# Performance work log

Hardware: AMD Instinct MI355X
Metric: run time of the kernel (lower is better)

Reference implementation:

```python
import jax, jax.numpy as jnp
import numpy as np

SR = 44100
K = 1.0 / SR                      # time step
LX = 0.5
MAX_OM = 10000.0 * 2.0 * np.pi    # fmax * 2pi
MIN_OM = 20.0 * 2.0 * np.pi
TAU0, TAU1 = 6.0, 1.0
OM2SQ = (2.0 * np.pi * 500.0) ** 2          # OmDamp2^2 (OmDamp1 = 0)
ALPHA = 3.0 * np.log(10.0) / OM2SQ * (OM2SQ / TAU0)   # = 3 ln10 / tau0
BETA = 3.0 * np.log(10.0) / OM2SQ * (1.0 / TAU1 - 1.0 / TAU0)
MU_SCALE, DMU_SCALE, T0MU_SCALE = 2.43, 0.002452, 0.004115
M_MAX = 80  # 80x80 = 6400 modes


def setup_inputs() -> dict:
    z = jnp.zeros((), dtype=jnp.float32)
    return {
        "mu_raw": z, "D_over_mu_raw": z, "T0_over_mu_raw": z,
        "Ly_raw": z, "xo_raw": z, "yo_raw": z,
        "num_samples": 22050,
    }


def _modal_ir(mu_raw, D_over_mu_raw, T0_over_mu_raw, Ly_raw, xo_raw, yo_raw, num_samples):
    sp, sg = jax.nn.softplus, jax.nn.sigmoid
    # physical parameters via differentiable bounds
    mu = (sp(mu_raw) + 1e-4) * MU_SCALE
    D_over_mu = (sp(D_over_mu_raw) + 1e-4) * DMU_SCALE
    T0_over_mu = (sp(T0_over_mu_raw) + 1e-4) * T0MU_SCALE
    Ly = 1.1 + (4.0 - 1.1) * sg(Ly_raw)
    xo = 0.49 * LX + (1.0 - 0.49) * LX * sg(xo_raw)
    yo = 0.51 * Ly + (1.0 - 0.51) * Ly * sg(yo_raw)
    xi = 0.1 * LX
    yi = 0.1 * Ly
    # mode grid [6400]
    idx = jnp.arange(1, M_MAX + 1, dtype=jnp.float32)
    gm, gn = jnp.meshgrid(idx, idx, indexing="ij")
    m, n = gm.ravel(), gn.ravel()
    g1 = (m * np.pi / LX) ** 2 + (n * np.pi / Ly) ** 2
    omega_sq = T0_over_mu * g1 + D_over_mu * g1 * g1
    omega = jnp.sqrt(jax.nn.relu(omega_sq))
    valid = ((omega <= MAX_OM) & (omega >= MIN_OM)).astype(omega.dtype)
    InW = jnp.cos(xi * np.pi * m / LX) * jnp.cos(yi * np.pi * n / Ly)
    OutW = jnp.cos(xo * np.pi * m / LX) * jnp.cos(yo * np.pi * n / Ly)
    sigma = ALPHA + BETA * omega ** 2
    ms = 0.25 * mu * LX * Ly
    P = OutW * InW * (K * K) * jnp.exp(-sigma * K) / ms * valid  # [modes]
    # time axis [T]
    t = jnp.arange(num_samples, dtype=jnp.float32)
    decay_env = jnp.exp(-sigma[:, None] * (t[None, :] - 1.0) * K)    # [modes, T]
    sine_num = jnp.sin(t[None, :] * omega[:, None] * K)              # [modes, T]
    sine_den = jnp.sin(omega * K) + 1e-8                             # [modes]
    mode_waveforms = P[:, None] * decay_env * (sine_num / sine_den[:, None])
    disp = jnp.sum(mode_waveforms, axis=0)                           # [T]
    peak = jnp.max(jnp.abs(disp)) + 1e-8
    return disp / peak


def reference(mu_raw, D_over_mu_raw, T0_over_mu_raw, Ly_raw, xo_raw, yo_raw, num_samples):
    return _modal_ir(mu_raw, D_over_mu_raw, T0_over_mu_raw, Ly_raw, xo_raw, yo_raw, num_samples)
```

## Files before the change

kernel.cpp:

```cpp
#include <hip/hip_runtime.h>
#include <math.h>

#define NMODES 6400
#define TB     128
#define MPT    10
#define NPAIR  5
#define MG     5
#define BATCH  6
#define TC     42

typedef float v2f __attribute__((ext_vector_type(2)));

static __device__ __forceinline__ float softplusf(float x) {
    return log1pf(expf(-fabsf(x))) + fmaxf(x, 0.0f);
}
static __device__ __forceinline__ float sigmoidf(float x) {
    return 1.0f / (1.0f + expf(-x));
}

__global__ void setup_zero_kernel(const float* __restrict__ mu_raw,
                                  const float* __restrict__ Dmu_raw,
                                  const float* __restrict__ T0mu_raw,
                                  const float* __restrict__ Ly_raw,
                                  const float* __restrict__ xo_raw,
                                  const float* __restrict__ yo_raw,
                                  float* __restrict__ wsA,
                                  float* __restrict__ wsW,
                                  float* __restrict__ wsS,
                                  float* __restrict__ wsCW,
                                  float* __restrict__ wsSW,
                                  unsigned int* __restrict__ peak,
                                  float* __restrict__ out, int T)
{
    int id = blockIdx.x * blockDim.x + threadIdx.x;
    int gsz = gridDim.x * blockDim.x;
    for (int i = id; i < T; i += gsz) out[i] = 0.0f;
    if (id == 0) *peak = 0u;
    if (id >= NMODES) return;

    const float KF   = 1.0f / 44100.0f;
    const float PI_F = (float)M_PI;
    const double om2sq = (2.0 * M_PI * 500.0) * (2.0 * M_PI * 500.0);
    const float ALPHA_F  = (float)(3.0 * M_LN10 / om2sq * (om2sq / 6.0));
    const float BETA_F   = (float)(3.0 * M_LN10 / om2sq * (1.0 - 1.0 / 6.0));
    const float MAX_OM_F = (float)(10000.0 * 2.0 * M_PI);
    const float MIN_OM_F = (float)(20.0 * 2.0 * M_PI);
    const float KK_F     = (float)((1.0 / 44100.0) * (1.0 / 44100.0));

    float mu   = (softplusf(mu_raw[0])   + 1e-4f) * 2.43f;
    float Dmu  = (softplusf(Dmu_raw[0])  + 1e-4f) * 0.002452f;
    float T0mu = (softplusf(T0mu_raw[0]) + 1e-4f) * 0.004115f;
    float Ly   = 1.1f + 2.9f * sigmoidf(Ly_raw[0]);
    float xo   = 0.245f + 0.255f * sigmoidf(xo_raw[0]);
    float yo   = __fadd_rn(__fmul_rn(0.51f, Ly),
                           __fmul_rn(__fmul_rn(0.49f, Ly), sigmoidf(yo_raw[0])));

    float mf = (float)(id / 80 + 1);
    float nf = (float)(id % 80 + 1);

    float am = __fmul_rn(__fmul_rn(mf, PI_F), 2.0f);
    float bn = __fdiv_rn(__fmul_rn(nf, PI_F), Ly);
    float g1 = __fadd_rn(__fmul_rn(am, am), __fmul_rn(bn, bn));
    float omega_sq = __fadd_rn(__fmul_rn(T0mu, g1),
                               __fmul_rn(__fmul_rn(Dmu, g1), g1));
    float omega = sqrtf(fmaxf(omega_sq, 0.0f));
    float valid = (omega <= MAX_OM_F && omega >= MIN_OM_F) ? 1.0f : 0.0f;

    float xi_pi = (float)(0.05 * M_PI);
    float yi = __fmul_rn(0.1f, Ly);
    float InW = __fmul_rn(
        cosf(__fmul_rn(__fmul_rn(xi_pi, mf), 2.0f)),
        cosf(__fdiv_rn(__fmul_rn(__fmul_rn(yi, PI_F), nf), Ly)));
    float OutW = __fmul_rn(
        cosf(__fmul_rn(__fmul_rn(__fmul_rn(xo, PI_F), mf), 2.0f)),
        cosf(__fdiv_rn(__fmul_rn(__fmul_rn(yo, PI_F), nf), Ly)));

    float sigma = __fadd_rn(ALPHA_F, __fmul_rn(BETA_F, __fmul_rn(omega, omega)));
    float ms = __fmul_rn(__fmul_rn(__fmul_rn(0.25f, mu), 0.5f), Ly);
    float P = __fmul_rn(
        __fdiv_rn(__fmul_rn(__fmul_rn(__fmul_rn(OutW, InW), KK_F),
                            expf(__fmul_rn(-sigma, KF))),
                  ms),
        valid);
    float den = __fadd_rn(sinf(__fmul_rn(omega, KF)), 1e-8f);
    float A = __fdiv_rn(P, den);

    const double Kd = 1.0 / 44100.0;
    double th = (double)omega * Kd;
    double dd = exp(-(double)sigma * Kd);
    wsA[id]  = A;
    wsW[id]  = omega;
    wsS[id]  = sigma;
    wsCW[id] = (float)(dd * cos(th));
    wsSW[id] = (float)(dd * sin(th));
}

__global__ __launch_bounds__(TB) void accum_kernel(
    const float* __restrict__ wsA,
    const float* __restrict__ wsW,
    const float* __restrict__ wsS,
    const float* __restrict__ wsCW,
    const float* __restrict__ wsSW,
    float* __restrict__ out, int T)
{
    __shared__ __align__(16) float lds[TC][TB + 2];

    const int tid  = threadIdx.x;
    const int t0   = blockIdx.x * TC;
    const int base = blockIdx.y * (TB * MPT);

    const float  KF     = 1.0f / 44100.0f;
    const double Kd     = 1.0 / 44100.0;
    const double TWO_PI = 6.283185307179586476925286766559;
    const double I2PI   = 0.15915494309189533576888376337251;

    v2f S[NPAIR], C[NPAIR], CW[NPAIR], SW[NPAIR];
    #pragma unroll
    for (int p = 0; p < NPAIR; ++p) {
        int m = base + p * (TB * 2) + tid * 2;
        CW[p] = *(const v2f*)(wsCW + m);
        SW[p] = *(const v2f*)(wsSW + m);
        v2f A  = *(const v2f*)(wsA + m);
        v2f w  = *(const v2f*)(wsW + m);
        v2f sg = *(const v2f*)(wsS + m);
        #pragma unroll
        for (int k = 0; k < 2; ++k) {
            double ph = (double)t0 * (double)w[k] * Kd;
            double q  = rint(ph * I2PI);
            float  r  = (float)fma(-q, TWO_PI, ph);
            float s0, c0;
            __sincosf(r, &s0, &c0);
            float env = A[k] * __expf(-sg[k] * (float)(t0 - 1) * KF);
            S[p][k] = env * s0;
            C[p][k] = env * c0;
        }
    }

    #pragma unroll 1
    for (int it = 0; it < TC; it += BATCH) {
        #pragma unroll
        for (int b = 0; b < BATCH; ++b) {
            v2f s01 = S[0] + S[1];
            v2f s23 = S[2] + S[3];
            v2f sp  = (s01 + s23) + S[4];
            lds[it + b][tid] = sp[0] + sp[1];
            #pragma unroll
            for (int p = 0; p < NPAIR; ++p) {
                v2f nS = __builtin_elementwise_fma(S[p], CW[p], C[p] * SW[p]);
                v2f nC = __builtin_elementwise_fma(C[p], CW[p], -(S[p] * SW[p]));
                S[p] = nS;
                C[p] = nC;
            }
        }
    }
    __syncthreads();

    const int wv   = tid >> 6;
    const int lane = tid & 63;
    if (lane < TC / 2) {
        int s = wv * (TC / 2) + lane;
        v2f z = {0.0f, 0.0f};
        #pragma unroll
        for (int r = 0; r < TB / 2; ++r)
            z += *(const v2f*)&lds[s][2 * r];
        int t = t0 + s;
        if (t < T) atomicAdd(&out[t], z[0] + z[1]);
    }
}

__global__ __launch_bounds__(256) void max_kernel(
    const float* __restrict__ out,
    unsigned int* __restrict__ peak, int T)
{
    __shared__ float red[4];
    int i = blockIdx.x * 256 + threadIdx.x;
    float mx = 0.0f;
    if (2 * i + 1 < T) {
        v2f v = *(const v2f*)(out + 2 * i);
        mx = fmaxf(fabsf(v[0]), fabsf(v[1]));
    } else if (2 * i < T) {
        mx = fabsf(out[2 * i]);
    }
    #pragma unroll
    for (int off = 32; off > 0; off >>= 1)
        mx = fmaxf(mx, __shfl_xor(mx, off, 64));
    int lane = threadIdx.x & 63, wvx = threadIdx.x >> 6;
    if (lane == 0) red[wvx] = mx;
    __syncthreads();
    if (threadIdx.x == 0) {
        float m = fmaxf(fmaxf(red[0], red[1]), fmaxf(red[2], red[3]));
        atomicMax(peak, __float_as_uint(m));
    }
}

__global__ __launch_bounds__(256) void div_kernel(
    float* __restrict__ out, const unsigned int* __restrict__ peak, int T)
{
    float pk = __uint_as_float(*peak) + 1e-8f;
    int i = blockIdx.x * 256 + threadIdx.x;
    if (2 * i + 1 < T) {
        v2f v = *(const v2f*)(out + 2 * i);
        v[0] = __fdiv_rn(v[0], pk);
        v[1] = __fdiv_rn(v[1], pk);
        *(v2f*)(out + 2 * i) = v;
    } else if (2 * i < T) {
        out[2 * i] = __fdiv_rn(out[2 * i], pk);
    }
}

extern "C" void kernel_launch(void* const* d_in, const int* in_sizes, int n_in,
                              void* d_out, int out_size, void* d_ws, size_t ws_size,
                              hipStream_t stream)
{
    const float* mu   = (const float*)d_in[0];
    const float* Dmu  = (const float*)d_in[1];
    const float* T0mu = (const float*)d_in[2];
    const float* Lyr  = (const float*)d_in[3];
    const float* xor_ = (const float*)d_in[4];
    const float* yor_ = (const float*)d_in[5];
    float* out = (float*)d_out;

    float* ws   = (float*)d_ws;
    float* wsA  = ws;
    float* wsW  = ws + NMODES;
    float* wsS  = ws + 2 * NMODES;
    float* wsCW = ws + 3 * NMODES;
    float* wsSW = ws + 4 * NMODES;
    unsigned int* peak = (unsigned int*)(ws + 5 * NMODES);

    int T = out_size;
    int tchunks = (T + TC - 1) / TC;
    int npairs  = (T + 1) / 2;
    int nblk    = (npairs + 255) / 256;

    setup_zero_kernel<<<(NMODES + 255) / 256, 256, 0, stream>>>(
        mu, Dmu, T0mu, Lyr, xor_, yor_, wsA, wsW, wsS, wsCW, wsSW, peak, out, T);
    accum_kernel<<<dim3(tchunks, MG), TB, 0, stream>>>(wsA, wsW, wsS, wsCW, wsSW, out, T);
    max_kernel<<<nblk, 256, 0, stream>>>(out, peak, T);
    div_kernel<<<nblk, 256, 0, stream>>>(out, peak, T);
}
```

Baseline: 92.41 us.

## Fuse setup, accumulation, max and normalize into one cooperative kernel

Replaces the four separate launches (setup/zero, accumulate, max, divide) with a single cooperative persistent kernel using grid.sync between phases. The accumulate tiles (about 2625) are spread across a fixed 1024-block grid in a grid-stride loop. The aim is to remove per-launch overhead and the gaps between kernels. In exchange it adds grid-wide barriers and load imbalance, since the tile count does not divide evenly over 1024 blocks. Cooperative launch also requires all 1024 blocks to be resident at once.

```diff
diff --git a/kernel.cpp b/kernel.cpp
--- a/kernel.cpp
+++ b/kernel.cpp
@@ -1,4 +1,5 @@
 #include <hip/hip_runtime.h>
+#include <hip/hip_cooperative_groups.h>
 #include <math.h>
 
 #define NMODES 6400
@@ -8,6 +9,9 @@
 #define MG     5
 #define BATCH  6
 #define TC     42
+#define GRID   1024
+
+namespace cg = cooperative_groups;
 
 typedef float v2f __attribute__((ext_vector_type(2)));
 
@@ -18,193 +22,187 @@
     return 1.0f / (1.0f + expf(-x));
 }
 
-__global__ void setup_zero_kernel(const float* __restrict__ mu_raw,
-                                  const float* __restrict__ Dmu_raw,
-                                  const float* __restrict__ T0mu_raw,
-                                  const float* __restrict__ Ly_raw,
-                                  const float* __restrict__ xo_raw,
-                                  const float* __restrict__ yo_raw,
-                                  float* __restrict__ wsA,
-                                  float* __restrict__ wsW,
-                                  float* __restrict__ wsS,
-                                  float* __restrict__ wsCW,
-                                  float* __restrict__ wsSW,
-                                  unsigned int* __restrict__ peak,
-                                  float* __restrict__ out, int T)
-{
-    int id = blockIdx.x * blockDim.x + threadIdx.x;
-    int gsz = gridDim.x * blockDim.x;
-    for (int i = id; i < T; i += gsz) out[i] = 0.0f;
-    if (id == 0) *peak = 0u;
-    if (id >= NMODES) return;
-
-    const float KF   = 1.0f / 44100.0f;
-    const float PI_F = (float)M_PI;
-    const double om2sq = (2.0 * M_PI * 500.0) * (2.0 * M_PI * 500.0);
-    const float ALPHA_F  = (float)(3.0 * M_LN10 / om2sq * (om2sq / 6.0));
-    const float BETA_F   = (float)(3.0 * M_LN10 / om2sq * (1.0 - 1.0 / 6.0));
-    const float MAX_OM_F = (float)(10000.0 * 2.0 * M_PI);
-    const float MIN_OM_F = (float)(20.0 * 2.0 * M_PI);
-    const float KK_F     = (float)((1.0 / 44100.0) * (1.0 / 44100.0));
-
-    float mu   = (softplusf(mu_raw[0])   + 1e-4f) * 2.43f;
-    float Dmu  = (softplusf(Dmu_raw[0])  + 1e-4f) * 0.002452f;
-    float T0mu = (softplusf(T0mu_raw[0]) + 1e-4f) * 0.004115f;
-    float Ly   = 1.1f + 2.9f * sigmoidf(Ly_raw[0]);
-    float xo   = 0.245f + 0.255f * sigmoidf(xo_raw[0]);
-    float yo   = __fadd_rn(__fmul_rn(0.51f, Ly),
-                           __fmul_rn(__fmul_rn(0.49f, Ly), sigmoidf(yo_raw[0])));
-
-    float mf = (float)(id / 80 + 1);
-    float nf = (float)(id % 80 + 1);
-
-    float am = __fmul_rn(__fmul_rn(mf, PI_F), 2.0f);
-    float bn = __fdiv_rn(__fmul_rn(nf, PI_F), Ly);
-    float g1 = __fadd_rn(__fmul_rn(am, am), __fmul_rn(bn, bn));
-    float omega_sq = __fadd_rn(__fmul_rn(T0mu, g1),
-                               __fmul_rn(__fmul_rn(Dmu, g1), g1));
-    float omega = sqrtf(fmaxf(omega_sq, 0.0f));
-    float valid = (omega <= MAX_OM_F && omega >= MIN_OM_F) ? 1.0f : 0.0f;
-
-    float xi_pi = (float)(0.05 * M_PI);
-    float yi = __fmul_rn(0.1f, Ly);
-    float InW = __fmul_rn(
-        cosf(__fmul_rn(__fmul_rn(xi_pi, mf), 2.0f)),
-        cosf(__fdiv_rn(__fmul_rn(__fmul_rn(yi, PI_F), nf), Ly)));
-    float OutW = __fmul_rn(
-        cosf(__fmul_rn(__fmul_rn(__fmul_rn(xo, PI_F), mf), 2.0f)),
-        cosf(__fdiv_rn(__fmul_rn(__fmul_rn(yo, PI_F), nf), Ly)));
-
-    float sigma = __fadd_rn(ALPHA_F, __fmul_rn(BETA_F, __fmul_rn(omega, omega)));
-    float ms = __fmul_rn(__fmul_rn(__fmul_rn(0.25f, mu), 0.5f), Ly);
-    float P = __fmul_rn(
-        __fdiv_rn(__fmul_rn(__fmul_rn(__fmul_rn(OutW, InW), KK_F),
-                            expf(__fmul_rn(-sigma, KF))),
-                  ms),
-        valid);
-    float den = __fadd_rn(sinf(__fmul_rn(omega, KF)), 1e-8f);
-    float A = __fdiv_rn(P, den);
-
-    const double Kd = 1.0 / 44100.0;
-    double th = (double)omega * Kd;
-    double dd = exp(-(double)sigma * Kd);
-    wsA[id]  = A;
-    wsW[id]  = omega;
-    wsS[id]  = sigma;
-    wsCW[id] = (float)(dd * cos(th));
-    wsSW[id] = (float)(dd * sin(th));
-}
-
-__global__ __launch_bounds__(TB) void accum_kernel(
-    const float* __restrict__ wsA,
-    const float* __restrict__ wsW,
-    const float* __restrict__ wsS,
-    const float* __restrict__ wsCW,
-    const float* __restrict__ wsSW,
+__global__ __launch_bounds__(TB) void mega_kernel(
+    const float* __restrict__ mu_raw,
+    const float* __restrict__ Dmu_raw,
+    const float* __restrict__ T0mu_raw,
+    const float* __restrict__ Ly_raw,
+    const float* __restrict__ xo_raw,
+    const float* __restrict__ yo_raw,
+    float* __restrict__ wsA,
+    float* __restrict__ wsW,
+    float* __restrict__ wsS,
+    float* __restrict__ wsCW,
+    float* __restrict__ wsSW,
+    unsigned int* __restrict__ peak,
     float* __restrict__ out, int T)
 {
+    cg::grid_group grid = cg::this_grid();
     __shared__ __align__(16) float lds[TC][TB + 2];
-
-    const int tid  = threadIdx.x;
-    const int t0   = blockIdx.x * TC;
-    const int base = blockIdx.y * (TB * MPT);
+    __shared__ float red[2];
+
+    const int tid = threadIdx.x;
+    const int gt  = blockIdx.x * TB + tid;
+    const int GT  = gridDim.x * TB;
 
     const float  KF     = 1.0f / 44100.0f;
     const double Kd     = 1.0 / 44100.0;
     const double TWO_PI = 6.283185307179586476925286766559;
     const double I2PI   = 0.15915494309189533576888376337251;
 
-    v2f S[NPAIR], C[NPAIR], CW[NPAIR], SW[NPAIR];
-    #pragma unroll
-    for (int p = 0; p < NPAIR; ++p) {
-        int m = base + p * (TB * 2) + tid * 2;
-        CW[p] = *(const v2f*)(wsCW + m);
-        SW[p] = *(const v2f*)(wsSW + m);
-        v2f A  = *(const v2f*)(wsA + m);
-        v2f w  = *(const v2f*)(wsW + m);
-        v2f sg = *(const v2f*)(wsS + m);
+    for (int i = gt; i < T; i += GT) out[i] = 0.0f;
+    if (gt == 0) *peak = 0u;
+    if (gt < NMODES) {
+        const float PI_F = (float)M_PI;
+        const double om2sq = (2.0 * M_PI * 500.0) * (2.0 * M_PI * 500.0);
+        const float ALPHA_F  = (float)(3.0 * M_LN10 / om2sq * (om2sq / 6.0));
+        const float BETA_F   = (float)(3.0 * M_LN10 / om2sq * (1.0 - 1.0 / 6.0));
+        const float MAX_OM_F = (float)(10000.0 * 2.0 * M_PI);
+        const float MIN_OM_F = (float)(20.0 * 2.0 * M_PI);
+        const float KK_F     = (float)((1.0 / 44100.0) * (1.0 / 44100.0));
+
+        float mu   = (softplusf(mu_raw[0])   + 1e-4f) * 2.43f;
+        float Dmu  = (softplusf(Dmu_raw[0])  + 1e-4f) * 0.002452f;
+        float T0mu = (softplusf(T0mu_raw[0]) + 1e-4f) * 0.004115f;
+        float Ly   = 1.1f + 2.9f * sigmoidf(Ly_raw[0]);
+        float xo   = 0.245f + 0.255f * sigmoidf(xo_raw[0]);
+        float yo   = __fadd_rn(__fmul_rn(0.51f, Ly),
+                               __fmul_rn(__fmul_rn(0.49f, Ly), sigmoidf(yo_raw[0])));
+
+        float mf = (float)(gt / 80 + 1);
+        float nf = (float)(gt % 80 + 1);
+
+        float am = __fmul_rn(__fmul_rn(mf, PI_F), 2.0f);
+        float bn = __fdiv_rn(__fmul_rn(nf, PI_F), Ly);
+        float g1 = __fadd_rn(__fmul_rn(am, am), __fmul_rn(bn, bn));
+        float omega_sq = __fadd_rn(__fmul_rn(T0mu, g1),
+                                   __fmul_rn(__fmul_rn(Dmu, g1), g1));
+        float omega = sqrtf(fmaxf(omega_sq, 0.0f));
+        float valid = (omega <= MAX_OM_F && omega >= MIN_OM_F) ? 1.0f : 0.0f;
+
+        float xi_pi = (float)(0.05 * M_PI);
+        float yi = __fmul_rn(0.1f, Ly);
+        float InW = __fmul_rn(
+            cosf(__fmul_rn(__fmul_rn(xi_pi, mf), 2.0f)),
+            cosf(__fdiv_rn(__fmul_rn(__fmul_rn(yi, PI_F), nf), Ly)));
+        float OutW = __fmul_rn(
+            cosf(__fmul_rn(__fmul_rn(__fmul_rn(xo, PI_F), mf), 2.0f)),
+            cosf(__fdiv_rn(__fmul_rn(__fmul_rn(yo, PI_F), nf), Ly)));
+
+        float sigma = __fadd_rn(ALPHA_F, __fmul_rn(BETA_F, __fmul_rn(omega, omega)));
+        float ms = __fmul_rn(__fmul_rn(__fmul_rn(0.25f, mu), 0.5f), Ly);
+        float P = __fmul_rn(
+            __fdiv_rn(__fmul_rn(__fmul_rn(__fmul_rn(OutW, InW), KK_F),
+                                expf(__fmul_rn(-sigma, KF))),
+                      ms),
+            valid);
+        float den = __fadd_rn(sinf(__fmul_rn(omega, KF)), 1e-8f);
+        float A = __fdiv_rn(P, den);
+
+        double th = (double)omega * Kd;
+        double dd = exp(-(double)sigma * Kd);
+        wsA[gt]  = A;
+        wsW[gt]  = omega;
+        wsS[gt]  = sigma;
+        wsCW[gt] = (float)(dd * cos(th));
+        wsSW[gt] = (float)(dd * sin(th));
+    }
+    grid.sync();
+
+    const int tchunks = (T + TC - 1) / TC;
+    const int NT = tchunks * MG;
+    for (int tile = blockIdx.x; tile < NT; tile += gridDim.x) {
+        const int t0   = (tile % tchunks) * TC;
+        const int base = (tile / tchunks) * (TB * MPT);
+
+        v2f S[NPAIR], C[NPAIR], CW[NPAIR], SW[NPAIR];
         #pragma unroll
-        for (int k = 0; k < 2; ++k) {
-            double ph = (double)t0 * (double)w[k] * Kd;
-            double q  = rint(ph * I2PI);
-            float  r  = (float)fma(-q, TWO_PI, ph);
-            float s0, c0;
-            __sincosf(r, &s0, &c0);
-            float env = A[k] * __expf(-sg[k] * (float)(t0 - 1) * KF);
-            S[p][k] = env * s0;
-            C[p][k] = env * c0;
-        }
-    }
-
-    #pragma unroll 1
-    for (int it = 0; it < TC; it += BATCH) {
-        #pragma unroll
-        for (int b = 0; b < BATCH; ++b) {
-            v2f s01 = S[0] + S[1];
-            v2f s23 = S[2] + S[3];
-            v2f sp  = (s01 + s23) + S[4];
-            lds[it + b][tid] = sp[0] + sp[1];
+        for (int p = 0; p < NPAIR; ++p) {
+            int m = base + p * (TB * 2) + tid * 2;
+            CW[p] = *(const v2f*)(wsCW + m);
+            SW[p] = *(const v2f*)(wsSW + m);
+            v2f A  = *(const v2f*)(wsA + m);
+            v2f w  = *(const v2f*)(wsW + m);
+            v2f sg = *(const v2f*)(wsS + m);
             #pragma unroll
-            for (int p = 0; p < NPAIR; ++p) {
-                v2f nS = __builtin_elementwise_fma(S[p], CW[p], C[p] * SW[p]);
-                v2f nC = __builtin_elementwise_fma(C[p], CW[p], -(S[p] * SW[p]));
-                S[p] = nS;
-                C[p] = nC;
+            for (int k = 0; k < 2; ++k) {
+                double ph = (double)t0 * (double)w[k] * Kd;
+                double q  = rint(ph * I2PI);
+                float  r  = (float)fma(-q, TWO_PI, ph);
+                float s0, c0;
+                __sincosf(r, &s0, &c0);
+                float env = A[k] * __expf(-sg[k] * (float)(t0 - 1) * KF);
+                S[p][k] = env * s0;
+                C[p][k] = env * c0;
             }
         }
-    }
-    __syncthreads();
-
-    const int wv   = tid >> 6;
-    const int lane = tid & 63;
-    if (lane < TC / 2) {
-        int s = wv * (TC / 2) + lane;
-        v2f z = {0.0f, 0.0f};
-        #pragma unroll
-        for (int r = 0; r < TB / 2; ++r)
-            z += *(const v2f*)&lds[s][2 * r];
-        int t = t0 + s;
-        if (t < T) atomicAdd(&out[t], z[0] + z[1]);
-    }
-}
-
-__global__ __launch_bounds__(256) void max_kernel(
-    const float* __restrict__ out,
-    unsigned int* __restrict__ peak, int T)
-{
-    __shared__ float red[4];
-    int i = blockIdx.x * 256 + threadIdx.x;
+
+        #pragma unroll 1
+        for (int it = 0; it < TC; it += BATCH) {
+            #pragma unroll
+            for (int b = 0; b < BATCH; ++b) {
+                v2f s01 = S[0] + S[1];
+                v2f s23 = S[2] + S[3];
+                v2f sp  = (s01 + s23) + S[4];
+                lds[it + b][tid] = sp[0] + sp[1];
+                #pragma unroll
+                for (int p = 0; p < NPAIR; ++p) {
+                    v2f nS = __builtin_elementwise_fma(S[p], CW[p], C[p] * SW[p]);
+                    v2f nC = __builtin_elementwise_fma(C[p], CW[p], -(S[p] * SW[p]));
+                    S[p] = nS;
+                    C[p] = nC;
+                }
+            }
+        }
+        __syncthreads();
+
+        const int wv   = tid >> 6;
+        const int lane = tid & 63;
+        if (lane < TC / 2) {
+            int s = wv * (TC / 2) + lane;
+            v2f z = {0.0f, 0.0f};
+            #pragma unroll
+            for (int r = 0; r < TB / 2; ++r)
+                z += *(const v2f*)&lds[s][2 * r];
+            int t = t0 + s;
+            if (t < T) atomicAdd(&out[t], z[0] + z[1]);
+        }
+        __syncthreads();
+    }
+    grid.sync();
+
+    const int npairs = (T + 1) >> 1;
     float mx = 0.0f;
-    if (2 * i + 1 < T) {
-        v2f v = *(const v2f*)(out + 2 * i);
-        mx = fmaxf(fabsf(v[0]), fabsf(v[1]));
-    } else if (2 * i < T) {
-        mx = fabsf(out[2 * i]);
+    for (int i = gt; i < npairs; i += GT) {
+        if (2 * i + 1 < T) {
+            v2f v = *(const v2f*)(out + 2 * i);
+            mx = fmaxf(mx, fmaxf(fabsf(v[0]), fabsf(v[1])));
+        } else {
+            mx = fmaxf(mx, fabsf(out[2 * i]));
+        }
     }
     #pragma unroll
     for (int off = 32; off > 0; off >>= 1)
         mx = fmaxf(mx, __shfl_xor(mx, off, 64));
-    int lane = threadIdx.x & 63, wvx = threadIdx.x >> 6;
-    if (lane == 0) red[wvx] = mx;
+    if ((tid & 63) == 0) red[tid >> 6] = mx;
     __syncthreads();
-    if (threadIdx.x == 0) {
-        float m = fmaxf(fmaxf(red[0], red[1]), fmaxf(red[2], red[3]));
-        atomicMax(peak, __float_as_uint(m));
-    }
-}
-
-__global__ __launch_bounds__(256) void div_kernel(
-    float* __restrict__ out, const unsigned int* __restrict__ peak, int T)
-{
-    float pk = __uint_as_float(*peak) + 1e-8f;
-    int i = blockIdx.x * 256 + threadIdx.x;
-    if (2 * i + 1 < T) {
-        v2f v = *(const v2f*)(out + 2 * i);
-        v[0] = __fdiv_rn(v[0], pk);
-        v[1] = __fdiv_rn(v[1], pk);
-        *(v2f*)(out + 2 * i) = v;
-    } else if (2 * i < T) {
-        out[2 * i] = __fdiv_rn(out[2 * i], pk);
+    if (tid == 0) {
+        float m = fmaxf(red[0], red[1]);
+        if (m > 0.0f) atomicMax(peak, __float_as_uint(m));
+    }
+    grid.sync();
+
+    float pk = __uint_as_float(
+        __hip_atomic_load(peak, __ATOMIC_RELAXED, __HIP_MEMORY_SCOPE_AGENT)) + 1e-8f;
+    for (int i = gt; i < npairs; i += GT) {
+        if (2 * i + 1 < T) {
+            v2f v = *(const v2f*)(out + 2 * i);
+            v[0] = __fdiv_rn(v[0], pk);
+            v[1] = __fdiv_rn(v[1], pk);
+            *(v2f*)(out + 2 * i) = v;
+        } else {
+            out[2 * i] = __fdiv_rn(out[2 * i], pk);
+        }
     }
 }
 
@@ -229,13 +227,12 @@
     unsigned int* peak = (unsigned int*)(ws + 5 * NMODES);
 
     int T = out_size;
-    int tchunks = (T + TC - 1) / TC;
-    int npairs  = (T + 1) / 2;
-    int nblk    = (npairs + 255) / 256;
-
-    setup_zero_kernel<<<(NMODES + 255) / 256, 256, 0, stream>>>(
-        mu, Dmu, T0mu, Lyr, xor_, yor_, wsA, wsW, wsS, wsCW, wsSW, peak, out, T);
-    accum_kernel<<<dim3(tchunks, MG), TB, 0, stream>>>(wsA, wsW, wsS, wsCW, wsSW, out, T);
-    max_kernel<<<nblk, 256, 0, stream>>>(out, peak, T);
-    div_kernel<<<nblk, 256, 0, stream>>>(out, peak, T);
-}
+
+    void* args[] = {
+        (void*)&mu, (void*)&Dmu, (void*)&T0mu, (void*)&Lyr, (void*)&xor_,
+        (void*)&yor_, (void*)&wsA, (void*)&wsW, (void*)&wsS, (void*)&wsCW,
+        (void*)&wsSW, (void*)&peak, (void*)&out, (void*)&T
+    };
+    hipLaunchCooperativeKernel((void*)mega_kernel, dim3(GRID), dim3(TB),
+                               args, 0, stream);
+}
```

After: 360.0 us. 290% more time.

## Fuse peak-normalisation into accumulation kernel via last-block completion counter

Applied to the files above, without the earlier changes.

Drops the separate max and divide kernels. Each accumulation block increments a global completion counter, and the last block to finish computes the absolute peak and normalises the whole output. This is meant to remove two kernel launches and their gaps. In exchange, the final reduction and divide run serially in a single 128-thread block and add an atomic per block.

```diff
diff --git a/kernel.cpp b/kernel.cpp
--- a/kernel.cpp
+++ b/kernel.cpp
@@ -29,13 +29,13 @@
                                   float* __restrict__ wsS,
                                   float* __restrict__ wsCW,
                                   float* __restrict__ wsSW,
-                                  unsigned int* __restrict__ peak,
+                                  unsigned int* __restrict__ done,
                                   float* __restrict__ out, int T)
 {
     int id = blockIdx.x * blockDim.x + threadIdx.x;
     int gsz = gridDim.x * blockDim.x;
     for (int i = id; i < T; i += gsz) out[i] = 0.0f;
-    if (id == 0) *peak = 0u;
+    if (id == 0) *done = 0u;
     if (id >= NMODES) return;
 
     const float KF   = 1.0f / 44100.0f;
@@ -101,9 +101,12 @@
     const float* __restrict__ wsS,
     const float* __restrict__ wsCW,
     const float* __restrict__ wsSW,
-    float* __restrict__ out, int T)
+    float* out,
+    unsigned int* done, int T)
 {
     __shared__ __align__(16) float lds[TC][TB + 2];
+    __shared__ unsigned int isLast;
+    __shared__ float red2[2];
 
     const int tid  = threadIdx.x;
     const int t0   = blockIdx.x * TC;
@@ -166,45 +169,34 @@
         int t = t0 + s;
         if (t < T) atomicAdd(&out[t], z[0] + z[1]);
     }
-}
-
-__global__ __launch_bounds__(256) void max_kernel(
-    const float* __restrict__ out,
-    unsigned int* __restrict__ peak, int T)
-{
-    __shared__ float red[4];
-    int i = blockIdx.x * 256 + threadIdx.x;
-    float mx = 0.0f;
-    if (2 * i + 1 < T) {
-        v2f v = *(const v2f*)(out + 2 * i);
-        mx = fmaxf(fabsf(v[0]), fabsf(v[1]));
-    } else if (2 * i < T) {
-        mx = fabsf(out[2 * i]);
-    }
-    #pragma unroll
-    for (int off = 32; off > 0; off >>= 1)
-        mx = fmaxf(mx, __shfl_xor(mx, off, 64));
-    int lane = threadIdx.x & 63, wvx = threadIdx.x >> 6;
-    if (lane == 0) red[wvx] = mx;
     __syncthreads();
-    if (threadIdx.x == 0) {
-        float m = fmaxf(fmaxf(red[0], red[1]), fmaxf(red[2], red[3]));
-        atomicMax(peak, __float_as_uint(m));
-    }
-}
-
-__global__ __launch_bounds__(256) void div_kernel(
-    float* __restrict__ out, const unsigned int* __restrict__ peak, int T)
-{
-    float pk = __uint_as_float(*peak) + 1e-8f;
-    int i = blockIdx.x * 256 + threadIdx.x;
-    if (2 * i + 1 < T) {
-        v2f v = *(const v2f*)(out + 2 * i);
-        v[0] = __fdiv_rn(v[0], pk);
-        v[1] = __fdiv_rn(v[1], pk);
-        *(v2f*)(out + 2 * i) = v;
-    } else if (2 * i < T) {
-        out[2 * i] = __fdiv_rn(out[2 * i], pk);
+
+    if (tid == 0) {
+        __threadfence();
+        unsigned int old = atomicAdd(done, 1u);
+        unsigned int ntiles = gridDim.x * gridDim.y;
+        isLast = (old == ntiles - 1u) ? 1u : 0u;
+    }
+    __syncthreads();
+    if (isLast) {
+        __threadfence();
+        float mx = 0.0f;
+        for (int i = tid; i < T; i += TB) {
+            float v = __hip_atomic_load(&out[i], __ATOMIC_RELAXED,
+                                        __HIP_MEMORY_SCOPE_AGENT);
+            mx = fmaxf(mx, fabsf(v));
+        }
+        #pragma unroll
+        for (int off = 32; off > 0; off >>= 1)
+            mx = fmaxf(mx, __shfl_xor(mx, off, 64));
+        if (lane == 0) red2[wv] = mx;
+        __syncthreads();
+        float pk = fmaxf(red2[0], red2[1]) + 1e-8f;
+        for (int i = tid; i < T; i += TB) {
+            float v = __hip_atomic_load(&out[i], __ATOMIC_RELAXED,
+                                        __HIP_MEMORY_SCOPE_AGENT);
+            out[i] = __fdiv_rn(v, pk);
+        }
     }
 }
 
@@ -226,16 +218,13 @@
     float* wsS  = ws + 2 * NMODES;
     float* wsCW = ws + 3 * NMODES;
     float* wsSW = ws + 4 * NMODES;
-    unsigned int* peak = (unsigned int*)(ws + 5 * NMODES);
+    unsigned int* done = (unsigned int*)(ws + 5 * NMODES);
 
     int T = out_size;
     int tchunks = (T + TC - 1) / TC;
-    int npairs  = (T + 1) / 2;
-    int nblk    = (npairs + 255) / 256;
 
     setup_zero_kernel<<<(NMODES + 255) / 256, 256, 0, stream>>>(
-        mu, Dmu, T0mu, Lyr, xor_, yor_, wsA, wsW, wsS, wsCW, wsSW, peak, out, T);
-    accum_kernel<<<dim3(tchunks, MG), TB, 0, stream>>>(wsA, wsW, wsS, wsCW, wsSW, out, T);
-    max_kernel<<<nblk, 256, 0, stream>>>(out, peak, T);
-    div_kernel<<<nblk, 256, 0, stream>>>(out, peak, T);
-}
+        mu, Dmu, T0mu, Lyr, xor_, yor_, wsA, wsW, wsS, wsCW, wsSW, done, out, T);
+    accum_kernel<<<dim3(tchunks, MG), TB, 0, stream>>>(
+        wsA, wsW, wsS, wsCW, wsSW, out, done, T);
+}
```

New measurement: 188.5 us. +104.0%, slower.
